# Kernel optimization log

Hardware: AMD Instinct MI355X
Metric: run time of the kernel (lower is better)

Reference implementation:

```python
import jax, jax.numpy as jnp
import numpy as np

EPS_COS = 1e-8   # torch F.cosine_similarity eps
EPS_L1 = 1e-12   # torch F.normalize eps


def setup_inputs() -> dict:
    key = jax.random.key(0)
    k1, k2, k3, k4 = jax.random.split(key, 4)
    B, D, C = 32768, 768, 200
    features = jax.random.normal(k1, (B, D), dtype=jnp.float32)
    centers = jax.random.normal(k2, (C, D), dtype=jnp.float32)
    labels = jax.random.randint(k3, (B,), 0, C)
    labelled_or_not = jax.random.randint(k4, (B,), 0, 2).astype(jnp.bool_)
    return {"features": features, "centers": centers, "labels": labels,
            "labelled_or_not": labelled_or_not}


def reference(features, centers, labels, labelled_or_not):
    # cosine similarity: x.y / (max(|x|,eps) * max(|y|,eps))
    fn = features / jnp.maximum(jnp.linalg.norm(features, axis=1, keepdims=True), EPS_COS)
    cn = centers / jnp.maximum(jnp.linalg.norm(centers, axis=1, keepdims=True), EPS_COS)
    cos = jnp.einsum('bd,cd->bc', fn, cn)  # [B, C]

    # per-sample sign logic: label column -> +|cos|, all others -> -|cos|
    a = jnp.abs(cos)
    is_label = jax.nn.one_hot(labels, cos.shape[1], dtype=jnp.bool_)  # [B, C]
    signed = jnp.where(is_label, a, -a)

    # L1 normalize per row (||row||_1 == sum of |cos| regardless of signs)
    l1 = jnp.sum(a, axis=1, keepdims=True)
    normed = signed / jnp.maximum(l1, EPS_L1)

    # only labelled rows contribute (row-wise normalize is independent per row,
    # so masking after is equivalent to boolean-indexing before)
    contrib = jnp.where(labelled_or_not[:, None], normed, 0.0)
    return -jnp.sum(contrib)
```

## Files before the change

kernel.cpp:

```cpp
#include <hip/hip_runtime.h>
#include <hip/hip_bf16.h>

#define NROWS 32768
#define DIMS  768
#define NC    200
#define CPAD  256
#define KSTEP 32
#define NSTEP (DIMS / KSTEP)
#define ROWSB 64

typedef __attribute__((ext_vector_type(8))) short short8;
typedef __attribute__((ext_vector_type(4))) float f32x4;

#define WAITV4 asm volatile("s_waitcnt vmcnt(4)" ::: "memory")
#define WAITL0 asm volatile("s_waitcnt lgkmcnt(0)" ::: "memory")
#define BAR    __builtin_amdgcn_s_barrier()

__device__ __forceinline__ unsigned pk_bf16(float lo, float hi) {
  union { __hip_bfloat162 h; unsigned u; } c;
  c.h = __float22bfloat162_rn(make_float2(lo, hi));
  return c.u;
}

__global__ __launch_bounds__(256) void prep_centers_k(const float* __restrict__ centers,
                                                      short* __restrict__ cnb2,
                                                      float* __restrict__ out) {
  const int c = blockIdx.x;
  const int tid = threadIdx.x;
  if (c == 0 && tid == 0) out[0] = 0.f;
  if (c >= NC) {
    for (int d = tid; d < DIMS; d += 256)
      cnb2[(d >> 5) * (CPAD * KSTEP) + c * KSTEP + (d & 31)] = 0;
    return;
  }
  float ssq = 0.f;
  for (int d = tid; d < DIMS; d += 256) {
    float v = centers[c * DIMS + d];
    ssq += v * v;
  }
#pragma unroll
  for (int off = 32; off > 0; off >>= 1) ssq += __shfl_down(ssq, off);
  __shared__ float red[4];
  const int wid = tid >> 6, lane = tid & 63;
  if (lane == 0) red[wid] = ssq;
  __syncthreads();
  const float tot = red[0] + red[1] + red[2] + red[3];
  const float inv = 1.f / fmaxf(sqrtf(tot), 1e-8f);
  for (int d = tid; d < DIMS; d += 256) {
    const float v = centers[c * DIMS + d] * inv;
    union { __hip_bfloat16 h; short s; } cv;
    cv.h = __float2bfloat16(v);
    cnb2[(d >> 5) * (CPAD * KSTEP) + c * KSTEP + (d & 31)] = cv.s;
  }
}

__global__ __launch_bounds__(512, 4) void cos_loss_k(
    const float* __restrict__ feats,
    const short* __restrict__ cnb2,
    const int* __restrict__ labels,
    const int* __restrict__ labelled,
    float* __restrict__ out) {
  const int tid = threadIdx.x;
  const int wid = tid >> 6;
  const int lane = tid & 63;
  const int rowBase = blockIdx.x * ROWSB;

  __shared__ short As[2][ROWSB][32];
  __shared__ float invs[ROWSB];
  __shared__ float l1part[4][ROWSB];
  __shared__ float alpart[4][ROWSB];

  if (wid < 4) {
    const int m = lane & 15;
    const int kg = lane >> 4;
    const int rdq = (kg ^ ((m >> 1) & 3)) * 8;
    const short* bp = cnb2 + (size_t)(wid * 64 + m) * KSTEP + kg * 8;

    f32x4 acc[4][4];
#pragma unroll
    for (int mi = 0; mi < 4; ++mi)
#pragma unroll
      for (int ni = 0; ni < 4; ++ni) acc[mi][ni] = (f32x4){0.f, 0.f, 0.f, 0.f};

    short8 B[4];

#define BLOAD(ni, s) \
    B[ni] = *(const short8*)(bp + (size_t)(s) * (CPAD * KSTEP) + (ni) * (16 * KSTEP))

    BLOAD(0, 0); BLOAD(1, 0); BLOAD(2, 0); BLOAD(3, 0);
    BAR;

#define PHASEC(p, ab) do {                                               \
    const int sn_ = ((p) + 1 < NSTEP) ? (p) + 1 : NSTEP - 1;             \
    short8 af[4];                                                        \
    _Pragma("unroll")                                                    \
    for (int mi = 0; mi < 4; ++mi)                                       \
      af[mi] = *(const short8*)(&As[(ab)][mi * 16 + m][rdq]);            \
    __builtin_amdgcn_s_setprio(1);                                       \
    _Pragma("unroll")                                                    \
    for (int ni = 0; ni < 4; ++ni) {                                     \
      _Pragma("unroll")                                                  \
      for (int mi = 0; mi < 4; ++mi)                                     \
        acc[mi][ni] = __builtin_amdgcn_mfma_f32_16x16x32_bf16(           \
            af[mi], B[ni], acc[mi][ni], 0, 0, 0);                        \
      BLOAD(ni, sn_);                                                    \
    }                                                                    \
    __builtin_amdgcn_s_setprio(0);                                       \
    BAR;                                                                 \
  } while (0)

    for (int p = 0; p < NSTEP; p += 2) {
      PHASEC(p, 0);
      PHASEC(p + 1, 1);
    }
#undef BLOAD
#undef PHASEC

    BAR;

#pragma unroll
    for (int mi = 0; mi < 4; ++mi) {
      float l1r[4] = {0.f, 0.f, 0.f, 0.f};
      float alr[4] = {0.f, 0.f, 0.f, 0.f};
      float iv[4];
      int labr[4];
#pragma unroll
      for (int r = 0; r < 4; ++r) {
        const int row = mi * 16 + kg * 4 + r;
        iv[r] = invs[row];
        labr[r] = labels[rowBase + row];
      }
#pragma unroll
      for (int ni = 0; ni < 4; ++ni) {
        const int col = wid * 64 + ni * 16 + m;
#pragma unroll
        for (int r = 0; r < 4; ++r) {
          const float a = fabsf(acc[mi][ni][r] * iv[r]);
          l1r[r] += a;
          if (col == labr[r]) alr[r] += a;
        }
      }
#pragma unroll
      for (int r = 0; r < 4; ++r) {
#pragma unroll
        for (int off = 1; off < 16; off <<= 1) {
          l1r[r] += __shfl_xor(l1r[r], off);
          alr[r] += __shfl_xor(alr[r], off);
        }
      }
      if (m == 0) {
#pragma unroll
        for (int r = 0; r < 4; ++r) {
          l1part[wid][mi * 16 + kg * 4 + r] = l1r[r];
          alpart[wid][mi * 16 + kg * 4 + r] = alr[r];
        }
      }
    }
  } else {
    const int pt = (wid - 4) * 64 + lane;
    const int arow = pt >> 2;
    const int aq   = pt & 3;
    const int aswz = (arow >> 1) & 3;
    const float* asrc = feats + (size_t)(rowBase + arow) * DIMS + aq * 8;
    short* adst0 = &As[0][arow][(aq ^ aswz) * 8];
    short* adst1 = &As[1][arow][(aq ^ aswz) * 8];

    float ssq = 0.f;
    float4 S0lo, S0hi, S1lo, S1hi, S2lo, S2hi;

#define LOADA(P, s) do {                                                 \
    const float* ap_ = asrc + (s) * KSTEP;                               \
    P##lo = *(const float4*)(ap_);                                       \
    P##hi = *(const float4*)(ap_ + 4);                                   \
  } while (0)

#define WRITEA(P, dst, guard) do {                                       \
    if (guard) {                                                         \
      ssq += P##lo.x*P##lo.x + P##lo.y*P##lo.y                           \
           + P##lo.z*P##lo.z + P##lo.w*P##lo.w;                          \
      ssq += P##hi.x*P##hi.x + P##hi.y*P##hi.y                           \
           + P##hi.z*P##hi.z + P##hi.w*P##hi.w;                          \
    }                                                                    \
    union { short8 s8; unsigned u[4]; } p_;                              \
    p_.u[0] = pk_bf16(P##lo.x, P##lo.y);                                 \
    p_.u[1] = pk_bf16(P##lo.z, P##lo.w);                                 \
    p_.u[2] = pk_bf16(P##hi.x, P##hi.y);                                 \
    p_.u[3] = pk_bf16(P##hi.z, P##hi.w);                                 \
    *(short8*)(dst) = p_.s8;                                             \
  } while (0)

#define CLMP(x) (((x) < NSTEP) ? (x) : NSTEP - 1)
#define PHASEP(p, SL, SP, dst) do {                                      \
    LOADA(SL, CLMP((p) + 3));                                            \
    WAITV4;                                                              \
    WRITEA(SP, dst, (p) + 1 < NSTEP);                                    \
    WAITL0;                                                              \
    BAR;                                                                 \
  } while (0)

    LOADA(S0, 0);
    LOADA(S1, 1);
    LOADA(S2, 2);
    WAITV4;
    WRITEA(S0, adst0, true);
    WAITL0;
    BAR;

    for (int p = 0; p < NSTEP; p += 6) {
      PHASEP(p + 0, S0, S1, adst1);
      PHASEP(p + 1, S1, S2, adst0);
      PHASEP(p + 2, S2, S0, adst1);
      PHASEP(p + 3, S0, S1, adst0);
      PHASEP(p + 4, S1, S2, adst1);
      PHASEP(p + 5, S2, S0, adst0);
    }
#undef LOADA
#undef WRITEA
#undef PHASEP
#undef CLMP

    ssq += __shfl_xor(ssq, 1);
    ssq += __shfl_xor(ssq, 2);
    if ((lane & 3) == 0) invs[arow] = 1.f / fmaxf(sqrtf(ssq), 1e-8f);
    WAITL0;
    BAR;
  }

  __syncthreads();

  if (tid < ROWSB) {
    const float L = l1part[0][tid] + l1part[1][tid] + l1part[2][tid] + l1part[3][tid];
    const float A = alpart[0][tid] + alpart[1][tid] + alpart[2][tid] + alpart[3][tid];
    float c = labelled[rowBase + tid] ? (L - 2.f * A) / fmaxf(L, 1e-12f) : 0.f;
#pragma unroll
    for (int off = 1; off < 64; off <<= 1) c += __shfl_xor(c, off);
    if (tid == 0) atomicAdd(out, c);
  }
}

extern "C" void kernel_launch(void* const* d_in, const int* in_sizes, int n_in,
                              void* d_out, int out_size, void* d_ws, size_t ws_size,
                              hipStream_t stream) {
  const float* feats = (const float*)d_in[0];
  const float* centers = (const float*)d_in[1];
  const int* labels = (const int*)d_in[2];
  const int* labelled = (const int*)d_in[3];
  float* out = (float*)d_out;
  short* cnb2 = (short*)d_ws;

  prep_centers_k<<<CPAD, 256, 0, stream>>>(centers, cnb2, out);
  cos_loss_k<<<NROWS / ROWSB, 512, 0, stream>>>(feats, cnb2, labels, labelled, out);
}
```

Before: 36.14 us.

## Double the K step per barrier phase and reshape the feature prefetch pipeline

Each pipeline phase now covers 64 K elements instead of 32, so the compute waves run two MFMA sub-steps with two B register sets per barrier, which halves the number of barriers. The producer waves load 16 floats per thread, use a 2-deep register prefetch instead of 3-deep, and write a wider LDS row with a new XOR swizzle over 8 chunks. This reduces synchronisation overhead but uses more registers and shortens the prefetch distance measured in phases.

```diff
diff --git a/kernel.cpp b/kernel.cpp
--- a/kernel.cpp
+++ b/kernel.cpp
@@ -1,13 +1,14 @@
 #include <hip/hip_runtime.h>
 #include <hip/hip_bf16.h>
 
-#define NROWS 32768
-#define DIMS  768
-#define NC    200
-#define CPAD  256
-#define KSTEP 32
-#define NSTEP (DIMS / KSTEP)
-#define ROWSB 64
+#define NROWS  32768
+#define DIMS   768
+#define NC     200
+#define CPAD   256
+#define KSUB   32
+#define KSTEP2 64
+#define NSTEP2 (DIMS / KSTEP2)
+#define ROWSB  64
 
 typedef __attribute__((ext_vector_type(8))) short short8;
 typedef __attribute__((ext_vector_type(4))) float f32x4;
@@ -30,7 +31,7 @@
   if (c == 0 && tid == 0) out[0] = 0.f;
   if (c >= NC) {
     for (int d = tid; d < DIMS; d += 256)
-      cnb2[(d >> 5) * (CPAD * KSTEP) + c * KSTEP + (d & 31)] = 0;
+      cnb2[(d >> 5) * (CPAD * KSUB) + c * KSUB + (d & 31)] = 0;
     return;
   }
   float ssq = 0.f;
@@ -50,7 +51,7 @@
     const float v = centers[c * DIMS + d] * inv;
     union { __hip_bfloat16 h; short s; } cv;
     cv.h = __float2bfloat16(v);
-    cnb2[(d >> 5) * (CPAD * KSTEP) + c * KSTEP + (d & 31)] = cv.s;
+    cnb2[(d >> 5) * (CPAD * KSUB) + c * KSUB + (d & 31)] = cv.s;
   }
 }
 
@@ -65,7 +66,7 @@
   const int lane = tid & 63;
   const int rowBase = blockIdx.x * ROWSB;
 
-  __shared__ short As[2][ROWSB][32];
+  __shared__ short As[2][ROWSB][64];
   __shared__ float invs[ROWSB];
   __shared__ float l1part[4][ROWSB];
   __shared__ float alpart[4][ROWSB];
@@ -73,8 +74,10 @@
   if (wid < 4) {
     const int m = lane & 15;
     const int kg = lane >> 4;
-    const int rdq = (kg ^ ((m >> 1) & 3)) * 8;
-    const short* bp = cnb2 + (size_t)(wid * 64 + m) * KSTEP + kg * 8;
+    const int sw = m & 7;
+    const int o0 = ((kg ^ sw)) * 8;
+    const int o1 = ((kg ^ sw) ^ 4) * 8;
+    const short* bp = cnb2 + (size_t)(wid * 64 + m) * KSUB + kg * 8;
 
     f32x4 acc[4][4];
 #pragma unroll
@@ -82,38 +85,55 @@
 #pragma unroll
       for (int ni = 0; ni < 4; ++ni) acc[mi][ni] = (f32x4){0.f, 0.f, 0.f, 0.f};
 
-    short8 B[4];
-
-#define BLOAD(ni, s) \
-    B[ni] = *(const short8*)(bp + (size_t)(s) * (CPAD * KSTEP) + (ni) * (16 * KSTEP))
-
-    BLOAD(0, 0); BLOAD(1, 0); BLOAD(2, 0); BLOAD(3, 0);
+    short8 B0[4], B1[4];
+
+#define BLD0(ni, s) B0[ni] = *(const short8*)(bp + (size_t)(2*(s)    ) * (CPAD*KSUB) + (ni) * (16*KSUB))
+#define BLD1(ni, s) B1[ni] = *(const short8*)(bp + (size_t)(2*(s) + 1) * (CPAD*KSUB) + (ni) * (16*KSUB))
+
+    BLD0(0,0); BLD0(1,0); BLD0(2,0); BLD0(3,0);
+    BLD1(0,0); BLD1(1,0); BLD1(2,0); BLD1(3,0);
     BAR;
 
 #define PHASEC(p, ab) do {                                               \
-    const int sn_ = ((p) + 1 < NSTEP) ? (p) + 1 : NSTEP - 1;             \
+    const int sn_ = ((p) + 1 < NSTEP2) ? (p) + 1 : NSTEP2 - 1;           \
     short8 af[4];                                                        \
+                                                 \
     _Pragma("unroll")                                                    \
     for (int mi = 0; mi < 4; ++mi)                                       \
-      af[mi] = *(const short8*)(&As[(ab)][mi * 16 + m][rdq]);            \
+      af[mi] = *(const short8*)(&As[(ab)][mi * 16 + m][o0]);             \
     __builtin_amdgcn_s_setprio(1);                                       \
     _Pragma("unroll")                                                    \
     for (int ni = 0; ni < 4; ++ni) {                                     \
       _Pragma("unroll")                                                  \
       for (int mi = 0; mi < 4; ++mi)                                     \
         acc[mi][ni] = __builtin_amdgcn_mfma_f32_16x16x32_bf16(           \
-            af[mi], B[ni], acc[mi][ni], 0, 0, 0);                        \
-      BLOAD(ni, sn_);                                                    \
+            af[mi], B0[ni], acc[mi][ni], 0, 0, 0);                       \
+      BLD0(ni, sn_);                                                     \
+    }                                                                    \
+    __builtin_amdgcn_s_setprio(0);                                       \
+                                                 \
+    _Pragma("unroll")                                                    \
+    for (int mi = 0; mi < 4; ++mi)                                       \
+      af[mi] = *(const short8*)(&As[(ab)][mi * 16 + m][o1]);             \
+    __builtin_amdgcn_s_setprio(1);                                       \
+    _Pragma("unroll")                                                    \
+    for (int ni = 0; ni < 4; ++ni) {                                     \
+      _Pragma("unroll")                                                  \
+      for (int mi = 0; mi < 4; ++mi)                                     \
+        acc[mi][ni] = __builtin_amdgcn_mfma_f32_16x16x32_bf16(           \
+            af[mi], B1[ni], acc[mi][ni], 0, 0, 0);                       \
+      BLD1(ni, sn_);                                                     \
     }                                                                    \
     __builtin_amdgcn_s_setprio(0);                                       \
     BAR;                                                                 \
   } while (0)
 
-    for (int p = 0; p < NSTEP; p += 2) {
+    for (int p = 0; p < NSTEP2; p += 2) {
       PHASEC(p, 0);
       PHASEC(p + 1, 1);
     }
-#undef BLOAD
+#undef BLD0
+#undef BLD1
 #undef PHASEC
 
     BAR;
@@ -159,64 +179,63 @@
   } else {
     const int pt = (wid - 4) * 64 + lane;
     const int arow = pt >> 2;
-    const int aq   = pt & 3;
-    const int aswz = (arow >> 1) & 3;
-    const float* asrc = feats + (size_t)(rowBase + arow) * DIMS + aq * 8;
-    short* adst0 = &As[0][arow][(aq ^ aswz) * 8];
-    short* adst1 = &As[1][arow][(aq ^ aswz) * 8];
+    const int ac   = pt & 3;
+    const int rs   = arow & 7;
+    const int lq   = ac * 2;
+    const float* asrc = feats + (size_t)(rowBase + arow) * DIMS + ac * 16;
+    const int pq0 = (lq ^ rs) * 8;
+    const int pq1 = ((lq + 1) ^ rs) * 8;
 
     float ssq = 0.f;
-    float4 S0lo, S0hi, S1lo, S1hi, S2lo, S2hi;
+    float4 S0a, S0b, S0c, S0d, S1a, S1b, S1c, S1d;
 
 #define LOADA(P, s) do {                                                 \
-    const float* ap_ = asrc + (s) * KSTEP;                               \
-    P##lo = *(const float4*)(ap_);                                       \
-    P##hi = *(const float4*)(ap_ + 4);                                   \
+    const float* ap_ = asrc + (s) * KSTEP2;                              \
+    P##a = *(const float4*)(ap_);                                        \
+    P##b = *(const float4*)(ap_ + 4);                                    \
+    P##c = *(const float4*)(ap_ + 8);                                    \
+    P##d = *(const float4*)(ap_ + 12);                                   \
   } while (0)
 
-#define WRITEA(P, dst, guard) do {                                       \
+#define WRITEA(P, buf, guard) do {                                       \
     if (guard) {                                                         \
-      ssq += P##lo.x*P##lo.x + P##lo.y*P##lo.y                           \
-           + P##lo.z*P##lo.z + P##lo.w*P##lo.w;                          \
-      ssq += P##hi.x*P##hi.x + P##hi.y*P##hi.y                           \
-           + P##hi.z*P##hi.z + P##hi.w*P##hi.w;                          \
+      ssq += P##a.x*P##a.x + P##a.y*P##a.y + P##a.z*P##a.z + P##a.w*P##a.w; \
+      ssq += P##b.x*P##b.x + P##b.y*P##b.y + P##b.z*P##b.z + P##b.w*P##b.w; \
+      ssq += P##c.x*P##c.x + P##c.y*P##c.y + P##c.z*P##c.z + P##c.w*P##c.w; \
+      ssq += P##d.x*P##d.x + P##d.y*P##d.y + P##d.z*P##d.z + P##d.w*P##d.w; \
     }                                                                    \
-    union { short8 s8; unsigned u[4]; } p_;                              \
-    p_.u[0] = pk_bf16(P##lo.x, P##lo.y);                                 \
-    p_.u[1] = pk_bf16(P##lo.z, P##lo.w);                                 \
-    p_.u[2] = pk_bf16(P##hi.x, P##hi.y);                                 \
-    p_.u[3] = pk_bf16(P##hi.z, P##hi.w);                                 \
-    *(short8*)(dst) = p_.s8;                                             \
+    union { short8 s8; unsigned u[4]; } q0_, q1_;                        \
+    q0_.u[0] = pk_bf16(P##a.x, P##a.y); q0_.u[1] = pk_bf16(P##a.z, P##a.w); \
+    q0_.u[2] = pk_bf16(P##b.x, P##b.y); q0_.u[3] = pk_bf16(P##b.z, P##b.w); \
+    q1_.u[0] = pk_bf16(P##c.x, P##c.y); q1_.u[1] = pk_bf16(P##c.z, P##c.w); \
+    q1_.u[2] = pk_bf16(P##d.x, P##d.y); q1_.u[3] = pk_bf16(P##d.z, P##d.w); \
+    *(short8*)(&As[(buf)][arow][pq0]) = q0_.s8;                          \
+    *(short8*)(&As[(buf)][arow][pq1]) = q1_.s8;                          \
   } while (0)
 
-#define CLMP(x) (((x) < NSTEP) ? (x) : NSTEP - 1)
-#define PHASEP(p, SL, SP, dst) do {                                      \
-    LOADA(SL, CLMP((p) + 3));                                            \
-    WAITV4;                                                              \
-    WRITEA(SP, dst, (p) + 1 < NSTEP);                                    \
-    WAITL0;                                                              \
-    BAR;                                                                 \
-  } while (0)
+#define CLMP(x) (((x) < NSTEP2) ? (x) : NSTEP2 - 1)
 
     LOADA(S0, 0);
     LOADA(S1, 1);
-    LOADA(S2, 2);
     WAITV4;
-    WRITEA(S0, adst0, true);
+    WRITEA(S0, 0, true);
     WAITL0;
     BAR;
 
-    for (int p = 0; p < NSTEP; p += 6) {
-      PHASEP(p + 0, S0, S1, adst1);
-      PHASEP(p + 1, S1, S2, adst0);
-      PHASEP(p + 2, S2, S0, adst1);
-      PHASEP(p + 3, S0, S1, adst0);
-      PHASEP(p + 4, S1, S2, adst1);
-      PHASEP(p + 5, S2, S0, adst0);
+    for (int p = 0; p < NSTEP2; p += 2) {
+      LOADA(S0, CLMP(p + 2));
+      WAITV4;
+      WRITEA(S1, 1, (p + 1 < NSTEP2));
+      WAITL0;
+      BAR;
+      LOADA(S1, CLMP(p + 3));
+      WAITV4;
+      WRITEA(S0, 0, (p + 2 < NSTEP2));
+      WAITL0;
+      BAR;
     }
 #undef LOADA
 #undef WRITEA
-#undef PHASEP
 #undef CLMP
 
     ssq += __shfl_xor(ssq, 1);
```

Result: no change. 36.19 us (+0.1%).

## Double rows per block to 128 and reshape producer prefetch to two stages

Applied to the files above, without the earlier changes.

Each block now handles 128 feature rows instead of 64, so every loaded center tile (B fragments) is reused across eight MFMA row tiles instead of four, halving per-row center traffic from L2. Producer threads each load 16 floats per step instead of 8, and the pipeline goes from triple to double buffering in registers. Launch bounds drop from 4 to 2 blocks per CU to make room for the larger accumulator set. The cost is fewer resident blocks and fewer blocks in flight to hide global-load latency, and the shallower prefetch gives less lead time before each load is needed.

```diff
diff --git a/kernel.cpp b/kernel.cpp
--- a/kernel.cpp
+++ b/kernel.cpp
@@ -7,7 +7,7 @@
 #define CPAD  256
 #define KSTEP 32
 #define NSTEP (DIMS / KSTEP)
-#define ROWSB 64
+#define ROWSB 128
 
 typedef __attribute__((ext_vector_type(8))) short short8;
 typedef __attribute__((ext_vector_type(4))) float f32x4;
@@ -54,7 +54,7 @@
   }
 }
 
-__global__ __launch_bounds__(512, 4) void cos_loss_k(
+__global__ __launch_bounds__(512, 2) void cos_loss_k(
     const float* __restrict__ feats,
     const short* __restrict__ cnb2,
     const int* __restrict__ labels,
@@ -76,9 +76,9 @@
     const int rdq = (kg ^ ((m >> 1) & 3)) * 8;
     const short* bp = cnb2 + (size_t)(wid * 64 + m) * KSTEP + kg * 8;
 
-    f32x4 acc[4][4];
-#pragma unroll
-    for (int mi = 0; mi < 4; ++mi)
+    f32x4 acc[8][4];
+#pragma unroll
+    for (int mi = 0; mi < 8; ++mi)
 #pragma unroll
       for (int ni = 0; ni < 4; ++ni) acc[mi][ni] = (f32x4){0.f, 0.f, 0.f, 0.f};
 
@@ -92,15 +92,15 @@
 
 #define PHASEC(p, ab) do {                                               \
     const int sn_ = ((p) + 1 < NSTEP) ? (p) + 1 : NSTEP - 1;             \
-    short8 af[4];                                                        \
+    short8 af[8];                                                        \
     _Pragma("unroll")                                                    \
-    for (int mi = 0; mi < 4; ++mi)                                       \
+    for (int mi = 0; mi < 8; ++mi)                                       \
       af[mi] = *(const short8*)(&As[(ab)][mi * 16 + m][rdq]);            \
     __builtin_amdgcn_s_setprio(1);                                       \
     _Pragma("unroll")                                                    \
     for (int ni = 0; ni < 4; ++ni) {                                     \
       _Pragma("unroll")                                                  \
-      for (int mi = 0; mi < 4; ++mi)                                     \
+      for (int mi = 0; mi < 8; ++mi)                                     \
         acc[mi][ni] = __builtin_amdgcn_mfma_f32_16x16x32_bf16(           \
             af[mi], B[ni], acc[mi][ni], 0, 0, 0);                        \
       BLOAD(ni, sn_);                                                    \
@@ -119,7 +119,7 @@
     BAR;
 
 #pragma unroll
-    for (int mi = 0; mi < 4; ++mi) {
+    for (int mi = 0; mi < 8; ++mi) {
       float l1r[4] = {0.f, 0.f, 0.f, 0.f};
       float alr[4] = {0.f, 0.f, 0.f, 0.f};
       float iv[4];
@@ -158,70 +158,68 @@
     }
   } else {
     const int pt = (wid - 4) * 64 + lane;
-    const int arow = pt >> 2;
-    const int aq   = pt & 3;
-    const int aswz = (arow >> 1) & 3;
-    const float* asrc = feats + (size_t)(rowBase + arow) * DIMS + aq * 8;
-    short* adst0 = &As[0][arow][(aq ^ aswz) * 8];
-    short* adst1 = &As[1][arow][(aq ^ aswz) * 8];
+    const int arow = pt >> 1;
+    const int ah   = pt & 1;
+    const int rs   = (arow >> 1) & 3;
+    const int lq   = ah * 2;
+    const float* asrc = feats + (size_t)(rowBase + arow) * DIMS + ah * 16;
+    const int pq0 = (lq ^ rs) * 8;
+    const int pq1 = ((lq + 1) ^ rs) * 8;
 
     float ssq = 0.f;
-    float4 S0lo, S0hi, S1lo, S1hi, S2lo, S2hi;
+    float4 S0a, S0b, S0c, S0d, S1a, S1b, S1c, S1d;
 
 #define LOADA(P, s) do {                                                 \
     const float* ap_ = asrc + (s) * KSTEP;                               \
-    P##lo = *(const float4*)(ap_);                                       \
-    P##hi = *(const float4*)(ap_ + 4);                                   \
+    P##a = *(const float4*)(ap_);                                        \
+    P##b = *(const float4*)(ap_ + 4);                                    \
+    P##c = *(const float4*)(ap_ + 8);                                    \
+    P##d = *(const float4*)(ap_ + 12);                                   \
   } while (0)
 
-#define WRITEA(P, dst, guard) do {                                       \
+#define WRITEA(P, buf, guard) do {                                       \
     if (guard) {                                                         \
-      ssq += P##lo.x*P##lo.x + P##lo.y*P##lo.y                           \
-           + P##lo.z*P##lo.z + P##lo.w*P##lo.w;                          \
-      ssq += P##hi.x*P##hi.x + P##hi.y*P##hi.y                           \
-           + P##hi.z*P##hi.z + P##hi.w*P##hi.w;                          \
+      ssq += P##a.x*P##a.x + P##a.y*P##a.y + P##a.z*P##a.z + P##a.w*P##a.w; \
+      ssq += P##b.x*P##b.x + P##b.y*P##b.y + P##b.z*P##b.z + P##b.w*P##b.w; \
+      ssq += P##c.x*P##c.x + P##c.y*P##c.y + P##c.z*P##c.z + P##c.w*P##c.w; \
+      ssq += P##d.x*P##d.x + P##d.y*P##d.y + P##d.z*P##d.z + P##d.w*P##d.w; \
     }                                                                    \
-    union { short8 s8; unsigned u[4]; } p_;                              \
-    p_.u[0] = pk_bf16(P##lo.x, P##lo.y);                                 \
-    p_.u[1] = pk_bf16(P##lo.z, P##lo.w);                                 \
-    p_.u[2] = pk_bf16(P##hi.x, P##hi.y);                                 \
-    p_.u[3] = pk_bf16(P##hi.z, P##hi.w);                                 \
-    *(short8*)(dst) = p_.s8;                                             \
+    union { short8 s8; unsigned u[4]; } q0_, q1_;                        \
+    q0_.u[0] = pk_bf16(P##a.x, P##a.y); q0_.u[1] = pk_bf16(P##a.z, P##a.w); \
+    q0_.u[2] = pk_bf16(P##b.x, P##b.y); q0_.u[3] = pk_bf16(P##b.z, P##b.w); \
+    q1_.u[0] = pk_bf16(P##c.x, P##c.y); q1_.u[1] = pk_bf16(P##c.z, P##c.w); \
+    q1_.u[2] = pk_bf16(P##d.x, P##d.y); q1_.u[3] = pk_bf16(P##d.z, P##d.w); \
+    *(short8*)(&As[(buf)][arow][pq0]) = q0_.s8;                          \
+    *(short8*)(&As[(buf)][arow][pq1]) = q1_.s8;                          \
   } while (0)
 
 #define CLMP(x) (((x) < NSTEP) ? (x) : NSTEP - 1)
-#define PHASEP(p, SL, SP, dst) do {                                      \
-    LOADA(SL, CLMP((p) + 3));                                            \
-    WAITV4;                                                              \
-    WRITEA(SP, dst, (p) + 1 < NSTEP);                                    \
-    WAITL0;                                                              \
-    BAR;                                                                 \
-  } while (0)
 
     LOADA(S0, 0);
     LOADA(S1, 1);
-    LOADA(S2, 2);
     WAITV4;
-    WRITEA(S0, adst0, true);
+    WRITEA(S0, 0, true);
     WAITL0;
     BAR;
 
-    for (int p = 0; p < NSTEP; p += 6) {
-      PHASEP(p + 0, S0, S1, adst1);
-      PHASEP(p + 1, S1, S2, adst0);
-      PHASEP(p + 2, S2, S0, adst1);
-      PHASEP(p + 3, S0, S1, adst0);
-      PHASEP(p + 4, S1, S2, adst1);
-      PHASEP(p + 5, S2, S0, adst0);
+    for (int p = 0; p < NSTEP; p += 2) {
+      LOADA(S0, CLMP(p + 2));
+      WAITV4;
+      WRITEA(S1, 1, (p + 1 < NSTEP));
+      WAITL0;
+      BAR;
+      LOADA(S1, CLMP(p + 3));
+      WAITV4;
+      WRITEA(S0, 0, (p + 2 < NSTEP));
+      WAITL0;
+      BAR;
     }
 #undef LOADA
 #undef WRITEA
-#undef PHASEP
 #undef CLMP
 
     ssq += __shfl_xor(ssq, 1);
-    ssq += __shfl_xor(ssq, 2);
-    if ((lane & 3) == 0) invs[arow] = 1.f / fmaxf(sqrtf(ssq), 1e-8f);
+    if ((lane & 1) == 0) invs[arow] = 1.f / fmaxf(sqrtf(ssq), 1e-8f);
     WAITL0;
     BAR;
   }
@@ -234,7 +232,7 @@
     float c = labelled[rowBase + tid] ? (L - 2.f * A) / fmaxf(L, 1e-12f) : 0.f;
 #pragma unroll
     for (int off = 1; off < 64; off <<= 1) c += __shfl_xor(c, off);
-    if (tid == 0) atomicAdd(out, c);
+    if ((tid & 63) == 0) atomicAdd(out, c);
   }
 }
 
```

New measurement: 37.74 us. 4.4% more time.
